# Kernel tuning notes

Measured on AMD Instinct MI355X. Metric: run time of the kernel, lower is better.

Reference implementation:

```python
import jax, jax.numpy as jnp
import numpy as np

N_SLICES = 2  # init kwarg n_slices


def affine_grid_3d(theta, D, H, W):
    """torch.nn.functional.affine_grid for 5D output, align_corners=False.
    theta: [B,3,4]; returns grid [B,D,H,W,3] with last dim (x,y,z) ~ (W,H,D)."""
    xs = (jnp.arange(W, dtype=theta.dtype) + 0.5) * (2.0 / W) - 1.0
    ys = (jnp.arange(H, dtype=theta.dtype) + 0.5) * (2.0 / H) - 1.0
    zs = (jnp.arange(D, dtype=theta.dtype) + 0.5) * (2.0 / D) - 1.0
    zz, yy, xx = jnp.meshgrid(zs, ys, xs, indexing='ij')
    base = jnp.stack([xx, yy, zz, jnp.ones_like(xx)], axis=-1)  # [D,H,W,4]
    return jnp.einsum('bij,dhwj->bdhwi', theta, base)  # [B,D,H,W,3]


def grid_sample_3d_zeros(vol, grid):
    """torch.nn.functional.grid_sample, mode='bilinear' (trilinear for 5D),
    padding_mode='zeros', align_corners=False.
    vol: [B,C,D,H,W]; grid: [B,D,H,W,3] normalized xyz coords."""
    B, C, D, H, W = vol.shape
    ix = ((grid[..., 0] + 1.0) * W - 1.0) * 0.5
    iy = ((grid[..., 1] + 1.0) * H - 1.0) * 0.5
    iz = ((grid[..., 2] + 1.0) * D - 1.0) * 0.5
    ix0 = jnp.floor(ix); iy0 = jnp.floor(iy); iz0 = jnp.floor(iz)
    fx = ix - ix0; fy = iy - iy0; fz = iz - iz0

    def gather(v, z, y, x):  # v: [C,D,H,W], idx: [D,H,W] -> [C,D,H,W]
        return v[:, z, y, x]

    out = jnp.zeros((B, C, D, H, W), vol.dtype)
    for dz in (0, 1):
        for dy in (0, 1):
            for dx in (0, 1):
                xi = ix0 + dx; yi = iy0 + dy; zi = iz0 + dz
                w = (jnp.where(dx, fx, 1.0 - fx)
                     * jnp.where(dy, fy, 1.0 - fy)
                     * jnp.where(dz, fz, 1.0 - fz))
                valid = ((xi >= 0) & (xi < W) & (yi >= 0) & (yi < H)
                         & (zi >= 0) & (zi < D))
                xc = jnp.clip(xi, 0, W - 1).astype(jnp.int32)
                yc = jnp.clip(yi, 0, H - 1).astype(jnp.int32)
                zc = jnp.clip(zi, 0, D - 1).astype(jnp.int32)
                vals = jax.vmap(gather)(vol, zc, yc, xc)  # [B,C,D,H,W]
                out = out + vals * (w * valid)[:, None]
    return out


def skip_connector(x, b_grid_affines):
    B, C, SPAT, _ = x.shape
    # zero volume with the 2D slice stack placed at the central W-plane
    vol = jnp.zeros((B, C, SPAT, SPAT, SPAT), x.dtype).at[..., SPAT // 2].set(x)
    chunks = jnp.split(vol, N_SLICES, axis=1)
    outs = []
    for i in range(N_SLICES):
        aff = b_grid_affines[i].astype(jnp.float32)  # [B,4,4]
        # get_zooms: column norms of rotation block
        zooms = jnp.sqrt((aff[:, :3, :3] ** 2).sum(axis=1))  # [B,3]
        # rescale_rot_components_with_diag(aff, 1/zooms) == aff @ diag(1/zx,1/zy,1/zz,1)
        scale = jnp.concatenate([1.0 / zooms, jnp.ones((aff.shape[0], 1), aff.dtype)], axis=1)
        aff = aff * scale[:, None, :]
        theta = jnp.linalg.inv(aff)[:, :3, :]  # [B,3,4]
        grid = affine_grid_3d(theta, SPAT, SPAT, SPAT)
        outs.append(grid_sample_3d_zeros(chunks[i], grid))
    return jnp.concatenate(outs, axis=1)  # [B,C,SPAT,SPAT,SPAT]


def setup_inputs() -> dict:
    key = jax.random.key(0)
    k1, k2 = jax.random.split(key)
    B, C, SPAT = 2, 32, 96
    x = jax.random.normal(k1, (B, C, SPAT, SPAT), dtype=jnp.float32)
    # near-identity invertible homogeneous affines for the two views (SA, HLA)
    noise = 0.1 * jax.random.normal(k2, (2, B, 4, 4), dtype=jnp.float32)
    aff = jnp.eye(4, dtype=jnp.float32)[None, None] + noise
    aff = aff.at[..., 3, :].set(jnp.array([0.0, 0.0, 0.0, 1.0], dtype=jnp.float32))
    return {"x": x, "b_grid_affines": aff}


def reference(x, b_grid_affines):
    return skip_connector(x, b_grid_affines)
```

## Files before the change

kernel.cpp:

```cpp
#include <hip/hip_runtime.h>
#include <math.h>

#define SPAT  96
#define IMG   (SPAT*SPAT)
#define PLANE (SPAT*SPAT*SPAT)
#define HROWS 48
#define HCHUNK (HROWS*24)

__device__ inline void invert4(const float m[16], float inv[16]) {
    inv[0]  =  m[5]*m[10]*m[15] - m[5]*m[11]*m[14] - m[9]*m[6]*m[15] + m[9]*m[7]*m[14] + m[13]*m[6]*m[11] - m[13]*m[7]*m[10];
    inv[4]  = -m[4]*m[10]*m[15] + m[4]*m[11]*m[14] + m[8]*m[6]*m[15] - m[8]*m[7]*m[14] - m[12]*m[6]*m[11] + m[12]*m[7]*m[10];
    inv[8]  =  m[4]*m[9]*m[15]  - m[4]*m[11]*m[13] - m[8]*m[5]*m[15] + m[8]*m[7]*m[13] + m[12]*m[5]*m[11] - m[12]*m[7]*m[9];
    inv[12] = -m[4]*m[9]*m[14]  + m[4]*m[10]*m[13] + m[8]*m[5]*m[14] - m[8]*m[6]*m[13] - m[12]*m[5]*m[10] + m[12]*m[6]*m[9];
    inv[1]  = -m[1]*m[10]*m[15] + m[1]*m[11]*m[14] + m[9]*m[2]*m[15] - m[9]*m[3]*m[14] - m[13]*m[2]*m[11] + m[13]*m[3]*m[10];
    inv[5]  =  m[0]*m[10]*m[15] - m[0]*m[11]*m[14] - m[8]*m[2]*m[15] + m[8]*m[3]*m[14] + m[12]*m[2]*m[11] - m[12]*m[3]*m[10];
    inv[9]  = -m[0]*m[9]*m[15]  + m[0]*m[11]*m[13] + m[8]*m[1]*m[15] - m[8]*m[3]*m[13] - m[12]*m[1]*m[11] + m[12]*m[3]*m[9];
    inv[13] =  m[0]*m[9]*m[14]  - m[0]*m[10]*m[13] - m[8]*m[1]*m[14] + m[8]*m[2]*m[13] + m[12]*m[1]*m[10] - m[12]*m[2]*m[9];
    inv[2]  =  m[1]*m[6]*m[15]  - m[1]*m[7]*m[14]  - m[5]*m[2]*m[15] + m[5]*m[3]*m[14] + m[13]*m[2]*m[7]  - m[13]*m[3]*m[6];
    inv[6]  = -m[0]*m[6]*m[15]  + m[0]*m[7]*m[14]  + m[4]*m[2]*m[15] - m[4]*m[3]*m[14] - m[12]*m[2]*m[7]  + m[12]*m[3]*m[6];
    inv[10] =  m[0]*m[5]*m[15]  - m[0]*m[7]*m[13]  - m[4]*m[1]*m[15] + m[4]*m[3]*m[13] + m[12]*m[1]*m[7]  - m[12]*m[3]*m[5];
    inv[14] = -m[0]*m[5]*m[14]  + m[0]*m[6]*m[13]  + m[4]*m[1]*m[14] - m[4]*m[2]*m[13] - m[12]*m[1]*m[6]  + m[12]*m[2]*m[5];
    inv[3]  = -m[1]*m[6]*m[11]  + m[1]*m[7]*m[10]  + m[5]*m[2]*m[11] - m[5]*m[3]*m[10] - m[9]*m[2]*m[7]   + m[9]*m[3]*m[6];
    inv[7]  =  m[0]*m[6]*m[11]  - m[0]*m[7]*m[10]  - m[4]*m[2]*m[11] + m[4]*m[3]*m[10] + m[8]*m[2]*m[7]   - m[8]*m[3]*m[6];
    inv[11] = -m[0]*m[5]*m[11]  + m[0]*m[7]*m[9]   + m[4]*m[1]*m[11] - m[4]*m[3]*m[9]  - m[8]*m[1]*m[7]   + m[8]*m[3]*m[5];
    inv[15] =  m[0]*m[5]*m[10]  - m[0]*m[6]*m[9]   - m[4]*m[1]*m[10] + m[4]*m[2]*m[9]  + m[8]*m[1]*m[6]   - m[8]*m[2]*m[5];
    float det  = m[0]*inv[0] + m[1]*inv[4] + m[2]*inv[8] + m[3]*inv[12];
    float rdet = 1.0f / det;
    for (int i = 0; i < 16; ++i) inv[i] *= rdet;
}

__global__ __launch_bounds__(256, 4) void fused4_kernel(
        const float* __restrict__ xin,
        const float* __restrict__ aff_in,
        float4* __restrict__ out) {
    __shared__ float4 tile[HCHUNK];
    const int tid = (int)threadIdx.x;
    const int dh2 = blockIdx.x;
    const int d   = dh2 >> 1;
    const int hh  = dh2 & 1;
    const int cc  = blockIdx.y;
    const int b   = cc >> 5;
    const int s   = (cc >> 4) & 1;
    const int sb  = s * 2 + b;

    float M[12];
    {
        float A[16];
        #pragma unroll
        for (int i = 0; i < 16; ++i) A[i] = aff_in[sb * 16 + i];
        #pragma unroll
        for (int j = 0; j < 3; ++j) {
            float z = sqrtf(A[0*4+j]*A[0*4+j] + A[1*4+j]*A[1*4+j] + A[2*4+j]*A[2*4+j]);
            float rz = 1.0f / z;
            #pragma unroll
            for (int i = 0; i < 4; ++i) A[i*4+j] *= rz;
        }
        float inv[16];
        invert4(A, inv);
        #pragma unroll
        for (int r = 0; r < 3; ++r) {
            float T0 = inv[r*4+0], T1 = inv[r*4+1], T2 = inv[r*4+2], T3 = inv[r*4+3];
            M[r*4+0] = T0;
            M[r*4+1] = T1;
            M[r*4+2] = T2;
            M[r*4+3] = -47.5f * (T0 + T1 + T2) + 48.0f * T3 + 47.5f;
        }
    }
    const float Mxw = M[0], Mxh = M[1], Mxd = M[2],  Mx0 = M[3];
    const float Myw = M[4], Myh = M[5], Myd = M[6],  My0 = M[7];
    const float Mzw = M[8], Mzh = M[9], Mzd = M[10], Mz0 = M[11];

    const float* img = xin + (size_t)cc * IMG;

    float tv[16];
    float bx = 0.f, by = 0.f, bz = 0.f;
    int   rr = 0, myq = 0, fqlo = 0, fqhi = -1;
    bool  act = false;
    if (tid < 2 * HROWS) {
        rr = tid >> 1;
        const int k = tid & 1;
        const int h = hh * HROWS + rr;
        const float fh = (float)h, fd = (float)d;
        bx = Mxh * fh + Mxd * fd + Mx0;
        by = Myh * fh + Myd * fd + My0;
        bz = Mzh * fh + Mzd * fd + Mz0;

        int wlo, whi;
        if (fabsf(Mxw) > 1e-6f) {
            float rMxw = 1.0f / Mxw;
            float w1 = (47.0f - bx) * rMxw;
            float w2 = (49.0f - bx) * rMxw;
            float wmin = fminf(w1, w2), wmax = fmaxf(w1, w2);
            wlo = max((int)ceilf(wmin), 0);
            whi = min((int)floorf(wmax), SPAT - 1);
        } else {
            bool in = fabsf(bx - 48.0f) < 1.0f;
            wlo = in ? 0 : 1;
            whi = in ? SPAT - 1 : 0;
        }
        const int qlo = wlo >> 2, qhi = whi >> 2;
        myq = qlo + k;
        if (wlo <= whi && myq <= qhi) {
            act = true;
            #pragma unroll
            for (int j = 0; j < 4; ++j) {
                float fw = (float)(4 * myq + j);
                float ix = Mxw * fw + bx;
                float wx = 1.0f - fabsf(ix - 48.0f);
                if (wx > 0.0f) {
                    float iy = Myw * fw + by;
                    float iz = Mzw * fw + bz;
                    int y0 = (int)floorf(iy), z0 = (int)floorf(iz);
                    int y0c = min(max(y0, 0),     SPAT - 1);
                    int y1c = min(max(y0 + 1, 0), SPAT - 1);
                    int z0c = min(max(z0, 0),     SPAT - 1);
                    int z1c = min(max(z0 + 1, 0), SPAT - 1);
                    tv[4*j+0] = img[z0c * SPAT + y0c];
                    tv[4*j+1] = img[z0c * SPAT + y1c];
                    tv[4*j+2] = img[z1c * SPAT + y0c];
                    tv[4*j+3] = img[z1c * SPAT + y1c];
                } else {
                    tv[4*j+0] = 0.f; tv[4*j+1] = 0.f;
                    tv[4*j+2] = 0.f; tv[4*j+3] = 0.f;
                }
            }
        }
        if (k == 1 && wlo <= whi) { fqlo = qlo + 2; fqhi = qhi; }
    }

    const float4 z4 = make_float4(0.f, 0.f, 0.f, 0.f);
    #pragma unroll
    for (int i = tid; i < HCHUNK; i += 256) tile[i] = z4;

    __syncthreads();

    if (act) {
        float vv[4];
        #pragma unroll
        for (int j = 0; j < 4; ++j) {
            float fw = (float)(4 * myq + j);
            float ix = Mxw * fw + bx;
            float wx = 1.0f - fabsf(ix - 48.0f);
            float r = 0.0f;
            if (wx > 0.0f) {
                float iy = Myw * fw + by;
                float iz = Mzw * fw + bz;
                float yf = floorf(iy), zf = floorf(iz);
                float fy = iy - yf,    fz = iz - zf;
                int y0 = (int)yf, z0 = (int)zf;
                bool vy0 = (y0 >= 0)  & (y0 <  SPAT);
                bool vy1 = (y0 >= -1) & (y0 <  SPAT - 1);
                bool vz0 = (z0 >= 0)  & (z0 <  SPAT);
                bool vz1 = (z0 >= -1) & (z0 <  SPAT - 1);
                float wy0 = 1.0f - fy, wy1 = fy;
                float wz0 = 1.0f - fz, wz1 = fz;
                float w00 = wx * wz0 * wy0 * ((vz0 & vy0) ? 1.0f : 0.0f);
                float w01 = wx * wz0 * wy1 * ((vz0 & vy1) ? 1.0f : 0.0f);
                float w10 = wx * wz1 * wy0 * ((vz1 & vy0) ? 1.0f : 0.0f);
                float w11 = wx * wz1 * wy1 * ((vz1 & vy1) ? 1.0f : 0.0f);
                r = w00 * tv[4*j+0] + w01 * tv[4*j+1]
                  + w10 * tv[4*j+2] + w11 * tv[4*j+3];
            }
            vv[j] = r;
        }
        tile[rr * 24 + myq] = make_float4(vv[0], vv[1], vv[2], vv[3]);
    }
    for (int q = fqlo; q <= fqhi; ++q) {
        float vv[4];
        #pragma unroll
        for (int j = 0; j < 4; ++j) {
            float fw = (float)(4 * q + j);
            float ix = Mxw * fw + bx;
            float wx = 1.0f - fabsf(ix - 48.0f);
            float r = 0.0f;
            if (wx > 0.0f) {
                float iy = Myw * fw + by;
                float iz = Mzw * fw + bz;
                float yf = floorf(iy), zf = floorf(iz);
                float fy = iy - yf,    fz = iz - zf;
                int y0 = (int)yf, z0 = (int)zf;
                bool vy0 = (y0 >= 0)  & (y0 <  SPAT);
                bool vy1 = (y0 >= -1) & (y0 <  SPAT - 1);
                bool vz0 = (z0 >= 0)  & (z0 <  SPAT);
                bool vz1 = (z0 >= -1) & (z0 <  SPAT - 1);
                int y0c = min(max(y0, 0),     SPAT - 1);
                int y1c = min(max(y0 + 1, 0), SPAT - 1);
                int z0c = min(max(z0, 0),     SPAT - 1);
                int z1c = min(max(z0 + 1, 0), SPAT - 1);
                float wy0 = 1.0f - fy, wy1 = fy;
                float wz0 = 1.0f - fz, wz1 = fz;
                float w00 = wx * wz0 * wy0 * ((vz0 & vy0) ? 1.0f : 0.0f);
                float w01 = wx * wz0 * wy1 * ((vz0 & vy1) ? 1.0f : 0.0f);
                float w10 = wx * wz1 * wy0 * ((vz1 & vy0) ? 1.0f : 0.0f);
                float w11 = wx * wz1 * wy1 * ((vz1 & vy1) ? 1.0f : 0.0f);
                r = w00 * img[z0c * SPAT + y0c] + w01 * img[z0c * SPAT + y1c]
                  + w10 * img[z1c * SPAT + y0c] + w11 * img[z1c * SPAT + y1c];
            }
            vv[j] = r;
        }
        tile[rr * 24 + q] = make_float4(vv[0], vv[1], vv[2], vv[3]);
    }

    __syncthreads();

    float4* op = out + ((size_t)cc * (PLANE / 4) + (size_t)d * (IMG / 4)
                        + (size_t)hh * HCHUNK);
    #pragma unroll
    for (int i = tid; i < HCHUNK; i += 256) op[i] = tile[i];
}

extern "C" void kernel_launch(void* const* d_in, const int* in_sizes, int n_in,
                              void* d_out, int out_size, void* d_ws, size_t ws_size,
                              hipStream_t stream) {
    const float* x   = (const float*)d_in[0];
    const float* aff = (const float*)d_in[1];
    float* out = (float*)d_out;

    dim3 grid(2 * SPAT, 64);
    fused4_kernel<<<grid, 256, 0, stream>>>(x, aff, (float4*)out);
}
```

Baseline: 220.3 us.

## Split into sparse prep kernel and flat streaming writer kernel using workspace

Adds a two-kernel path. A prep kernel computes the few non-zero float4 chunks per output row (the slab near the central plane) into a compact staging buffer with per-row range info. A grid-stride stream kernel then writes the whole output, filling zeros or staged values. The goal is to separate the gather-heavy sparse work from the bandwidth-bound full-volume write so the write runs at full coalesced throughput. The cost is a second launch, extra workspace traffic, and per-element integer division. The path is only used if the workspace is large enough; otherwise the old fused kernel runs.

```diff
diff --git a/kernel.cpp b/kernel.cpp
--- a/kernel.cpp
+++ b/kernel.cpp
@@ -4,6 +4,15 @@
 #define SPAT  96
 #define IMG   (SPAT*SPAT)
 #define PLANE (SPAT*SPAT*SPAT)
+#define CC_CH (PLANE/4)
+#define D_CH  (IMG/4)
+#define NCHUNK (64u*CC_CH)
+#define KSLOT 3
+#define STAGE_F4 (4*16*IMG*KSLOT)
+#define STAGE_BYTES ((size_t)STAGE_F4*16)
+#define NROWS (4*IMG)
+#define WS_NEED (STAGE_BYTES + (size_t)NROWS*4)
+
 #define HROWS 48
 #define HCHUNK (HROWS*24)
 
@@ -29,6 +38,169 @@
     for (int i = 0; i < 16; ++i) inv[i] *= rdet;
 }
 
+__device__ inline void fold_affine(const float* __restrict__ aff_in, int sb,
+                                   float M[12]) {
+    float A[16];
+    #pragma unroll
+    for (int i = 0; i < 16; ++i) A[i] = aff_in[sb * 16 + i];
+    #pragma unroll
+    for (int j = 0; j < 3; ++j) {
+        float z = sqrtf(A[0*4+j]*A[0*4+j] + A[1*4+j]*A[1*4+j] + A[2*4+j]*A[2*4+j]);
+        float rz = 1.0f / z;
+        #pragma unroll
+        for (int i = 0; i < 4; ++i) A[i*4+j] *= rz;
+    }
+    float inv[16];
+    invert4(A, inv);
+    #pragma unroll
+    for (int r = 0; r < 3; ++r) {
+        float T0 = inv[r*4+0], T1 = inv[r*4+1], T2 = inv[r*4+2], T3 = inv[r*4+3];
+        M[r*4+0] = T0;
+        M[r*4+1] = T1;
+        M[r*4+2] = T2;
+        M[r*4+3] = -47.5f * (T0 + T1 + T2) + 48.0f * T3 + 47.5f;
+    }
+}
+
+__global__ __launch_bounds__(128) void prep_kernel(
+        const float* __restrict__ xin,
+        const float* __restrict__ aff_in,
+        float4* __restrict__ stage,
+        unsigned* __restrict__ rowinfo,
+        float* __restrict__ outp) {
+    const int tid = (int)threadIdx.x;
+    if (tid >= SPAT) return;
+    const int d  = blockIdx.x;
+    const int sb = blockIdx.y;
+    const int h  = tid;
+
+    float M[12];
+    fold_affine(aff_in, sb, M);
+    const float Mxw = M[0], Mxh = M[1], Mxd = M[2],  Mx0 = M[3];
+    const float Myw = M[4], Myh = M[5], Myd = M[6],  My0 = M[7];
+    const float Mzw = M[8], Mzh = M[9], Mzd = M[10], Mz0 = M[11];
+
+    const float fh = (float)h, fd = (float)d;
+    const float bx = Mxh * fh + Mxd * fd + Mx0;
+
+    int wlo, whi;
+    if (fabsf(Mxw) > 1e-6f) {
+        float rMxw = 1.0f / Mxw;
+        float w1 = (47.0f - bx) * rMxw;
+        float w2 = (49.0f - bx) * rMxw;
+        float wmin = fminf(w1, w2), wmax = fmaxf(w1, w2);
+        wlo = max((int)ceilf(wmin), 0);
+        whi = min((int)floorf(wmax), SPAT - 1);
+    } else {
+        bool in = fabsf(bx - 48.0f) < 1.0f;
+        wlo = in ? 0 : 1;
+        whi = in ? SPAT - 1 : 0;
+    }
+
+    const int rix = (sb * SPAT + d) * SPAT + h;
+    if (wlo > whi) { rowinfo[rix] = 0xFFu; return; }
+    const int qlo = wlo >> 2, qhi = whi >> 2;
+    const bool ovf = (qhi - qlo + 1) > KSLOT;
+    rowinfo[rix] = (unsigned)qlo | ((unsigned)qhi << 8) | (ovf ? 0x10000u : 0u);
+
+    const int s = sb >> 1, b = sb & 1;
+    const float* imgbase = xin + (size_t)(b * 32 + s * 16) * IMG;
+    const float by = Myh * fh + Myd * fd + My0;
+    const float bz = Mzh * fh + Mzd * fd + Mz0;
+
+    for (int q = qlo; q <= qhi; ++q) {
+        float wt[4][4];
+        int   of[4][4];
+        #pragma unroll
+        for (int j = 0; j < 4; ++j) {
+            float fw = (float)(4 * q + j);
+            float ix = Mxw * fw + bx;
+            float wx = 1.0f - fabsf(ix - 48.0f);
+            if (wx > 0.0f) {
+                float iy = Myw * fw + by;
+                float iz = Mzw * fw + bz;
+                float yf = floorf(iy), zf = floorf(iz);
+                float fy = iy - yf,    fz = iz - zf;
+                int y0 = (int)yf, z0 = (int)zf;
+                bool vy0 = (y0 >= 0)  & (y0 <  SPAT);
+                bool vy1 = (y0 >= -1) & (y0 <  SPAT - 1);
+                bool vz0 = (z0 >= 0)  & (z0 <  SPAT);
+                bool vz1 = (z0 >= -1) & (z0 <  SPAT - 1);
+                int y0c = min(max(y0, 0),     SPAT - 1);
+                int y1c = min(max(y0 + 1, 0), SPAT - 1);
+                int z0c = min(max(z0, 0),     SPAT - 1);
+                int z1c = min(max(z0 + 1, 0), SPAT - 1);
+                float wy0 = 1.0f - fy, wy1 = fy;
+                float wz0 = 1.0f - fz, wz1 = fz;
+                wt[j][0] = wx * wz0 * wy0 * ((vz0 & vy0) ? 1.0f : 0.0f);
+                wt[j][1] = wx * wz0 * wy1 * ((vz0 & vy1) ? 1.0f : 0.0f);
+                wt[j][2] = wx * wz1 * wy0 * ((vz1 & vy0) ? 1.0f : 0.0f);
+                wt[j][3] = wx * wz1 * wy1 * ((vz1 & vy1) ? 1.0f : 0.0f);
+                of[j][0] = z0c * SPAT + y0c;  of[j][1] = z0c * SPAT + y1c;
+                of[j][2] = z1c * SPAT + y0c;  of[j][3] = z1c * SPAT + y1c;
+            } else {
+                wt[j][0] = wt[j][1] = wt[j][2] = wt[j][3] = 0.0f;
+                of[j][0] = of[j][1] = of[j][2] = of[j][3] = 0;
+            }
+        }
+        if (!ovf) {
+            const int k = q - qlo;
+            #pragma unroll
+            for (int ct = 0; ct < 16; ++ct) {
+                const float* ic = imgbase + (size_t)ct * IMG;
+                float4 v;
+                v.x = wt[0][0]*ic[of[0][0]] + wt[0][1]*ic[of[0][1]] + wt[0][2]*ic[of[0][2]] + wt[0][3]*ic[of[0][3]];
+                v.y = wt[1][0]*ic[of[1][0]] + wt[1][1]*ic[of[1][1]] + wt[1][2]*ic[of[1][2]] + wt[1][3]*ic[of[1][3]];
+                v.z = wt[2][0]*ic[of[2][0]] + wt[2][1]*ic[of[2][1]] + wt[2][2]*ic[of[2][2]] + wt[2][3]*ic[of[2][3]];
+                v.w = wt[3][0]*ic[of[3][0]] + wt[3][1]*ic[of[3][1]] + wt[3][2]*ic[of[3][2]] + wt[3][3]*ic[of[3][3]];
+                stage[((size_t)(sb * 16 + ct) * IMG + (size_t)d * SPAT + h) * KSLOT + k] = v;
+            }
+        } else {
+            #pragma unroll
+            for (int ct = 0; ct < 16; ++ct) {
+                const float* ic = imgbase + (size_t)ct * IMG;
+                float4 v;
+                v.x = wt[0][0]*ic[of[0][0]] + wt[0][1]*ic[of[0][1]] + wt[0][2]*ic[of[0][2]] + wt[0][3]*ic[of[0][3]];
+                v.y = wt[1][0]*ic[of[1][0]] + wt[1][1]*ic[of[1][1]] + wt[1][2]*ic[of[1][2]] + wt[1][3]*ic[of[1][3]];
+                v.z = wt[2][0]*ic[of[2][0]] + wt[2][1]*ic[of[2][1]] + wt[2][2]*ic[of[2][2]] + wt[2][3]*ic[of[2][3]];
+                v.w = wt[3][0]*ic[of[3][0]] + wt[3][1]*ic[of[3][1]] + wt[3][2]*ic[of[3][2]] + wt[3][3]*ic[of[3][3]];
+                *reinterpret_cast<float4*>(outp
+                    + (size_t)(b * 32 + s * 16 + ct) * PLANE
+                    + ((size_t)d * SPAT + h) * SPAT + 4 * q) = v;
+            }
+        }
+    }
+}
+
+__global__ __launch_bounds__(256) void stream_kernel(
+        const float4* __restrict__ stage,
+        const unsigned* __restrict__ rowinfo,
+        float4* __restrict__ out) {
+    size_t i = (size_t)blockIdx.x * 256 + threadIdx.x;
+    const size_t stride = (size_t)gridDim.x * 256;
+    for (; i < (size_t)NCHUNK; i += stride) {
+        unsigned ii = (unsigned)i;
+        unsigned cc = ii / CC_CH;
+        unsigned r1 = ii - cc * CC_CH;
+        unsigned dd = r1 / D_CH;
+        unsigned r2 = r1 - dd * D_CH;
+        unsigned hh = r2 / 24u;
+        unsigned q  = r2 - hh * 24u;
+        unsigned sb = ((cc >> 4) & 1u) * 2u + (cc >> 5);
+        unsigned info = rowinfo[(sb * SPAT + dd) * SPAT + hh];
+        unsigned qlo = info & 0xFFu;
+        unsigned qhi = (info >> 8) & 0xFFu;
+        bool ins = (q >= qlo) && (q <= qhi);
+        bool ovf = (info >> 16) != 0u;
+        float4 v = make_float4(0.f, 0.f, 0.f, 0.f);
+        if (ins && !ovf)
+            v = stage[((size_t)(sb * 16u + (cc & 15u)) * IMG
+                       + (size_t)dd * SPAT + hh) * KSLOT + (q - qlo)];
+        if (!(ins && ovf))
+            out[i] = v;
+    }
+}
+
 __global__ __launch_bounds__(256, 4) void fused4_kernel(
         const float* __restrict__ xin,
         const float* __restrict__ aff_in,
@@ -44,28 +216,7 @@
     const int sb  = s * 2 + b;
 
     float M[12];
-    {
-        float A[16];
-        #pragma unroll
-        for (int i = 0; i < 16; ++i) A[i] = aff_in[sb * 16 + i];
-        #pragma unroll
-        for (int j = 0; j < 3; ++j) {
-            float z = sqrtf(A[0*4+j]*A[0*4+j] + A[1*4+j]*A[1*4+j] + A[2*4+j]*A[2*4+j]);
-            float rz = 1.0f / z;
-            #pragma unroll
-            for (int i = 0; i < 4; ++i) A[i*4+j] *= rz;
-        }
-        float inv[16];
-        invert4(A, inv);
-        #pragma unroll
-        for (int r = 0; r < 3; ++r) {
-            float T0 = inv[r*4+0], T1 = inv[r*4+1], T2 = inv[r*4+2], T3 = inv[r*4+3];
-            M[r*4+0] = T0;
-            M[r*4+1] = T1;
-            M[r*4+2] = T2;
-            M[r*4+3] = -47.5f * (T0 + T1 + T2) + 48.0f * T3 + 47.5f;
-        }
-    }
+    fold_affine(aff_in, sb, M);
     const float Mxw = M[0], Mxh = M[1], Mxd = M[2],  Mx0 = M[3];
     const float Myw = M[4], Myh = M[5], Myd = M[6],  My0 = M[7];
     const float Mzw = M[8], Mzh = M[9], Mzd = M[10], Mz0 = M[11];
@@ -216,6 +367,14 @@
     const float* aff = (const float*)d_in[1];
     float* out = (float*)d_out;
 
-    dim3 grid(2 * SPAT, 64);
-    fused4_kernel<<<grid, 256, 0, stream>>>(x, aff, (float4*)out);
-}
+    if (d_ws != nullptr && ws_size >= WS_NEED) {
+        float4*   stage   = (float4*)d_ws;
+        unsigned* rowinfo = (unsigned*)((char*)d_ws + STAGE_BYTES);
+        dim3 pgrid(SPAT, 4);
+        prep_kernel<<<pgrid, 128, 0, stream>>>(x, aff, stage, rowinfo, out);
+        stream_kernel<<<4096, 256, 0, stream>>>(stage, rowinfo, (float4*)out);
+    } else {
+        dim3 grid(2 * SPAT, 64);
+        fused4_kernel<<<grid, 256, 0, stream>>>(x, aff, (float4*)out);
+    }
+}
```

Measured after the change: 255.9 us. 16.2% more time.
